# Kernel optimization log

Hardware: AMD Instinct MI355X
Metric: run time of the kernel (lower is better)

Reference implementation:

```python
import jax, jax.numpy as jnp
import numpy as np

B, T, I, H = 64, 512, 1024, 1024


def setup_inputs() -> dict:
    key = jax.random.key(0)
    k1, k2, k3, k4 = jax.random.split(key, 4)
    s_in = 1.0 / np.sqrt(I)
    s_h = 1.0 / np.sqrt(H)
    return {
        "x": jax.random.normal(k1, (B, T, I), dtype=jnp.float32),
        "Wih": jax.random.normal(k2, (4 * H, I), dtype=jnp.float32) * s_in,
        "Whh": jax.random.normal(k3, (4 * H, H), dtype=jnp.float32) * s_h,
        "b": jax.random.normal(k4, (4 * H,), dtype=jnp.float32) * s_h,
    }


def reference(x, Wih, Whh, b):
    """Sequential RNN layer (LSTM cell step) over (batch, seq_len, input).

    Mirrors RNNLayer.forward_tensor: zero-initialized state, per-timestep
    step(), stacked outputs plus final state. The Python time loop is
    expressed as a single lax.scan (one fused launch).
    """
    batch = x.shape[0]
    h0 = jnp.zeros((batch, H), dtype=x.dtype)
    c0 = jnp.zeros((batch, H), dtype=x.dtype)

    def step(carry, xt):  # xt: [B, I]
        h, c = carry
        gates = xt @ Wih.T + h @ Whh.T + b  # [B, 4H]
        i_g, f_g, g_g, o_g = jnp.split(gates, 4, axis=-1)
        c_new = jax.nn.sigmoid(f_g) * c + jax.nn.sigmoid(i_g) * jnp.tanh(g_g)
        h_new = jax.nn.sigmoid(o_g) * jnp.tanh(c_new)
        return (h_new, c_new), h_new

    xs = jnp.swapaxes(x, 0, 1)  # [T, B, I] for scan over time
    (h_T, c_T), outs = jax.lax.scan(step, (h0, c0), xs)
    outputs = jnp.swapaxes(outs, 0, 1)  # [B, T, H]
    return outputs, (h_T, c_T)
```

## Files before the change

kernel.cpp:

```cpp
#include <hip/hip_runtime.h>
#include <stdint.h>


typedef __bf16 bf16x8 __attribute__((ext_vector_type(8)));
typedef float f32x4 __attribute__((ext_vector_type(4)));

#define BATCH 64
#define TSEQ 512
#define HID 1024
#define MROWS (BATCH * TSEQ)
#define NGATE 4096

__device__ __forceinline__ unsigned short f2bf(float f) {
  union { float f; unsigned u; } v; v.f = f;
  unsigned r = (v.u + 0x7FFFu + ((v.u >> 16) & 1u)) >> 16;
  return (unsigned short)r;
}
__device__ __forceinline__ float bf2f(unsigned short u) {
  union { unsigned u; float f; } v; v.u = ((unsigned)u) << 16;
  return v.f;
}

__global__ void cvt_kernel(const float* __restrict__ src,
                           unsigned short* __restrict__ dst, int n4) {
  int i = blockIdx.x * blockDim.x + threadIdx.x;
  const int stride = gridDim.x * blockDim.x;
  for (; i < n4; i += stride) {
    float4 f = ((const float4*)src)[i];
    ushort4 u;
    u.x = f2bf(f.x); u.y = f2bf(f.y); u.z = f2bf(f.z); u.w = f2bf(f.w);
    ((ushort4*)dst)[i] = u;
  }
}

__device__ __forceinline__ void gl_lds16(const unsigned short* g, unsigned short* lds) {
  __builtin_amdgcn_global_load_lds(
      (const __attribute__((address_space(1))) unsigned int*)g,
      (__attribute__((address_space(3))) unsigned int*)lds, 16, 0, 0);
}

__global__ __launch_bounds__(256, 2) void gemm_xg(
    const unsigned short* __restrict__ A,
    const unsigned short* __restrict__ B,
    const float* __restrict__ bias,
    unsigned short* __restrict__ Xg)
{
  __shared__ __align__(16) unsigned short Asm[128 * 32];
  __shared__ __align__(16) unsigned short Bsm[128 * 32];
  const int tid = threadIdx.x;
  const int lane = tid & 63;
  const int wave = tid >> 6;
  const int row0 = blockIdx.y * 128;
  const int col0 = blockIdx.x * 128;
  const int wm = (wave >> 1) * 64;
  const int wn = (wave & 1) * 64;
  const int s_ml = lane >> 2;
  const int s_q = ((lane & 3) ^ (s_ml >> 1)) & 3;
  const int fm = lane & 15;
  const int fq = lane >> 4;
  const int swz = ((fq ^ (fm >> 1)) & 3) * 8;

  f32x4 acc[4][4] = {};

  for (int kt = 0; kt < 32; ++kt) {
    const int k0 = kt * 32;
    __syncthreads();
#pragma unroll
    for (int gI = 0; gI < 2; ++gI) {
      const int grp = wave * 2 + gI;
      const unsigned short* ga =
          A + (size_t)(row0 + grp * 16 + s_ml) * 1024 + k0 + s_q * 8;
      gl_lds16(ga, &Asm[grp * 512]);
      const unsigned short* gb =
          B + (size_t)(col0 + grp * 16 + s_ml) * 1024 + k0 + s_q * 8;
      gl_lds16(gb, &Bsm[grp * 512]);
    }
    __syncthreads();
    bf16x8 af[4], bfv[4];
#pragma unroll
    for (int mt = 0; mt < 4; ++mt) {
      const int m = wm + mt * 16 + fm;
      af[mt] = *(const bf16x8*)&Asm[(m >> 4) * 512 + fm * 32 + swz];
    }
#pragma unroll
    for (int nt = 0; nt < 4; ++nt) {
      const int n = wn + nt * 16 + fm;
      bfv[nt] = *(const bf16x8*)&Bsm[(n >> 4) * 512 + fm * 32 + swz];
    }
#pragma unroll
    for (int mt = 0; mt < 4; ++mt)
#pragma unroll
      for (int nt = 0; nt < 4; ++nt)
        acc[mt][nt] = __builtin_amdgcn_mfma_f32_16x16x32_bf16(
            af[mt], bfv[nt], acc[mt][nt], 0, 0, 0);
  }
#pragma unroll
  for (int nt = 0; nt < 4; ++nt) {
    const int nb = col0 + wn + nt * 16;
    const int pbase = ((nb & 1023) >> 4) * 64 + (nb >> 10) * 16;
    const float bv = bias[nb + fm];
#pragma unroll
    for (int mt = 0; mt < 4; ++mt) {
#pragma unroll
      for (int r = 0; r < 4; ++r) {
        const int row = row0 + wm + mt * 16 + fq * 4 + r;
        Xg[(size_t)row * 4096 + pbase + fm] = f2bf(acc[mt][nt][r] + bv);
      }
    }
  }
}

__device__ __forceinline__ bf16x8 load_h16B(const unsigned short* p) {
  union { unsigned long long q[2]; bf16x8 v; } u;
  const unsigned long long* q = (const unsigned long long*)p;
  u.q[0] = __hip_atomic_load(q, __ATOMIC_RELAXED, __HIP_MEMORY_SCOPE_AGENT);
  u.q[1] = __hip_atomic_load(q + 1, __ATOMIC_RELAXED, __HIP_MEMORY_SCOPE_AGENT);
  return u.v;
}

__global__ __launch_bounds__(256, 1) void lstm_seq(
    const unsigned short* __restrict__ Whh,
    const unsigned short* __restrict__ Xg,
    float* __restrict__ out,
    unsigned short* __restrict__ hbuf,
    unsigned int* __restrict__ flags)
{
  __shared__ float part[4][16][68];
  const int tid = threadIdx.x;
  const int lane = tid & 63;
  const int wave = tid >> 6;
  const int bn = blockIdx.x >> 2;
  const int mi = blockIdx.x & 3;
  const int fm = lane & 15;
  const int fq = lane >> 4;
  unsigned int* flg = flags + mi * 64 * 32;
  unsigned int* myflag = flg + bn * 32;
  unsigned int* pollp = flg + (wave * 16 + (lane & 15)) * 32;

  bf16x8 bfrag[4][8];
#pragma unroll
  for (int g = 0; g < 4; ++g) {
    const unsigned short* wrow =
        Whh + (size_t)(g * 1024 + bn * 16 + fm) * 1024 + wave * 256 + fq * 8;
#pragma unroll
    for (int ki = 0; ki < 8; ++ki) bfrag[g][ki] = *(const bf16x8*)(wrow + ki * 32);
  }

  const int em = tid >> 4, ej = tid & 15;
  const int gb = mi * 16 + em;
  const int gj = bn * 16 + ej;
  float c_reg = 0.f;

  unsigned short* h0 = hbuf;
  unsigned short* h1 = hbuf + BATCH * HID;

  const unsigned short* xrow = Xg + (size_t)gb * TSEQ * 4096 + bn * 64;
  float xpre[4];
#pragma unroll
  for (int g = 0; g < 4; ++g) xpre[g] = bf2f(xrow[g * 16 + ej]);

  for (int t = 0; t < TSEQ; ++t) {
    const unsigned short* hp = (t & 1) ? h1 : h0;
    unsigned short* hn = (t & 1) ? h0 : h1;
    const unsigned short* ab =
        hp + (size_t)(mi * 16 + fm) * 1024 + wave * 256 + fq * 8;

    float xcur[4];
#pragma unroll
    for (int g = 0; g < 4; ++g) xcur[g] = xpre[g];
    if (t < TSEQ - 1) {
      const unsigned short* xn = xrow + (size_t)(t + 1) * 4096;
#pragma unroll
      for (int g = 0; g < 4; ++g) xpre[g] = bf2f(xn[g * 16 + ej]);
    }

    if (t > 0) {
      for (;;) {
        const unsigned f = __hip_atomic_load(pollp, __ATOMIC_RELAXED,
                                             __HIP_MEMORY_SCOPE_AGENT);
        if (__all((int)(f >= (unsigned)t))) break;
        __builtin_amdgcn_s_sleep(1);
      }
      __builtin_amdgcn_sched_barrier(0);
    }

    bf16x8 afr[8];
#pragma unroll
    for (int ki = 0; ki < 8; ++ki) afr[ki] = load_h16B(ab + ki * 32);

    f32x4 acc[4] = {};
#pragma unroll
    for (int ki = 0; ki < 8; ++ki)
#pragma unroll
      for (int g = 0; g < 4; ++g)
        acc[g] = __builtin_amdgcn_mfma_f32_16x16x32_bf16(afr[ki], bfrag[g][ki],
                                                         acc[g], 0, 0, 0);

#pragma unroll
    for (int g = 0; g < 4; ++g)
#pragma unroll
      for (int r = 0; r < 4; ++r)
        part[wave][fq * 4 + r][g * 16 + fm] = acc[g][r];
    __syncthreads();

    float gate[4];
#pragma unroll
    for (int g = 0; g < 4; ++g) {
      float s = part[0][em][g * 16 + ej] + part[1][em][g * 16 + ej] +
                part[2][em][g * 16 + ej] + part[3][em][g * 16 + ej];
      gate[g] = s + xcur[g];
    }
    const float ig = 1.f / (1.f + __expf(-gate[0]));
    const float fg = 1.f / (1.f + __expf(-gate[1]));
    const float gg = 1.f - 2.f / (__expf(2.f * gate[2]) + 1.f);
    const float og = 1.f / (1.f + __expf(-gate[3]));
    c_reg = fg * c_reg + ig * gg;
    const float th = 1.f - 2.f / (__expf(2.f * c_reg) + 1.f);
    const float hv = og * th;

    __hip_atomic_store(&hn[(size_t)gb * HID + gj], f2bf(hv),
                       __ATOMIC_RELAXED, __HIP_MEMORY_SCOPE_AGENT);

    if (t == TSEQ - 1) {
      out[((size_t)gb * TSEQ + t) * HID + gj] = hv;
      out[(size_t)BATCH * TSEQ * HID + (size_t)gb * HID + gj] = hv;
      out[(size_t)BATCH * TSEQ * HID + (size_t)BATCH * HID + (size_t)gb * HID + gj] = c_reg;
      break;
    }

    __syncthreads();
    if (tid == 0)
      __hip_atomic_store(myflag, (unsigned)(t + 1),
                         __ATOMIC_RELAXED, __HIP_MEMORY_SCOPE_AGENT);

    out[((size_t)gb * TSEQ + t) * HID + gj] = hv;
  }
}

extern "C" void kernel_launch(void* const* d_in, const int* in_sizes, int n_in,
                              void* d_out, int out_size, void* d_ws, size_t ws_size,
                              hipStream_t stream) {
  (void)in_sizes; (void)n_in; (void)out_size;
  const float* x   = (const float*)d_in[0];
  const float* Wih = (const float*)d_in[1];
  const float* Whh = (const float*)d_in[2];
  const float* b   = (const float*)d_in[3];
  float* out = (float*)d_out;

  char* ws = (char*)d_ws;
  unsigned short* hbuf   = (unsigned short*)(ws + 1024);
  unsigned short* x_bf   = (unsigned short*)(ws + 263168);
  unsigned short* wih_bf = (unsigned short*)(ws + 263168 + 67108864);
  unsigned short* whh_bf = (unsigned short*)(ws + 263168 + 75497472);
  unsigned short* xg     = (unsigned short*)(ws + 263168 + 83886080);
  unsigned int* flags = (unsigned int*)x_bf;
  const size_t needed = 263168ULL + 83886080ULL + 268435456ULL;
  if (ws_size < needed) return;

  hipMemsetAsync(hbuf, 0, 2 * BATCH * HID * sizeof(unsigned short), stream);

  cvt_kernel<<<2048, 256, 0, stream>>>(x, x_bf, (MROWS * 1024) / 4);
  cvt_kernel<<<512, 256, 0, stream>>>(Wih, wih_bf, (NGATE * 1024) / 4);
  cvt_kernel<<<512, 256, 0, stream>>>(Whh, whh_bf, (NGATE * 1024) / 4);

  dim3 g(32, 256);
  gemm_xg<<<g, 256, 0, stream>>>(x_bf, wih_bf, b, xg);

  hipMemsetAsync(flags, 0, 4 * 64 * 128, stream);

  lstm_seq<<<256, 256, 0, stream>>>(whh_bf, xg, out, hbuf, flags);
}
```

Measured before the change: 2.235 ms.

## Use per-wave flags and double-buffered LDS to drop the second block barrier

Each wave now publishes its own progress flag once its h stores have drained (s_waitcnt vmcnt(0)). This replaces the second __syncthreads plus a single per-block flag. The partial-sum LDS buffer is double-buffered by step parity, so the next step's writes cannot race the previous step's reads without that barrier. The flags are packed densely, so each lane polls one flag instead of strided cache lines, and the s_sleep in the spin loop is removed. The changes aim to cut per-step synchronisation latency in the sequential recurrence. The cost is more polling traffic and contention, since dense flags share cache lines and the spin no longer sleeps.

```diff
diff --git a/kernel.cpp b/kernel.cpp
--- a/kernel.cpp
+++ b/kernel.cpp
@@ -125,7 +125,7 @@
     unsigned short* __restrict__ hbuf,
     unsigned int* __restrict__ flags)
 {
-  __shared__ float part[4][16][68];
+  __shared__ float part[2][4][16][68];
   const int tid = threadIdx.x;
   const int lane = tid & 63;
   const int wave = tid >> 6;
@@ -133,9 +133,9 @@
   const int mi = blockIdx.x & 3;
   const int fm = lane & 15;
   const int fq = lane >> 4;
-  unsigned int* flg = flags + mi * 64 * 32;
-  unsigned int* myflag = flg + bn * 32;
-  unsigned int* pollp = flg + (wave * 16 + (lane & 15)) * 32;
+  unsigned int* flg = flags + mi * 256;
+  unsigned int* myflag = flg + bn * 4 + wave;
+  unsigned int* pollp = flg + wave * 64 + lane;
 
   bf16x8 bfrag[4][8];
 #pragma unroll
@@ -175,11 +175,12 @@
     }
 
     if (t > 0) {
-      for (;;) {
-        const unsigned f = __hip_atomic_load(pollp, __ATOMIC_RELAXED,
-                                             __HIP_MEMORY_SCOPE_AGENT);
-        if (__all((int)(f >= (unsigned)t))) break;
-        __builtin_amdgcn_s_sleep(1);
+      const unsigned tt = (unsigned)t;
+      unsigned f = __hip_atomic_load(pollp, __ATOMIC_RELAXED,
+                                     __HIP_MEMORY_SCOPE_AGENT);
+      while (!__all((int)(f >= tt))) {
+        f = __hip_atomic_load(pollp, __ATOMIC_RELAXED,
+                              __HIP_MEMORY_SCOPE_AGENT);
       }
       __builtin_amdgcn_sched_barrier(0);
     }
@@ -196,18 +197,19 @@
         acc[g] = __builtin_amdgcn_mfma_f32_16x16x32_bf16(afr[ki], bfrag[g][ki],
                                                          acc[g], 0, 0, 0);
 
+    float (*pp)[16][68] = part[t & 1];
 #pragma unroll
     for (int g = 0; g < 4; ++g)
 #pragma unroll
       for (int r = 0; r < 4; ++r)
-        part[wave][fq * 4 + r][g * 16 + fm] = acc[g][r];
+        pp[wave][fq * 4 + r][g * 16 + fm] = acc[g][r];
     __syncthreads();
 
     float gate[4];
 #pragma unroll
     for (int g = 0; g < 4; ++g) {
-      float s = part[0][em][g * 16 + ej] + part[1][em][g * 16 + ej] +
-                part[2][em][g * 16 + ej] + part[3][em][g * 16 + ej];
+      float s = pp[0][em][g * 16 + ej] + pp[1][em][g * 16 + ej] +
+                pp[2][em][g * 16 + ej] + pp[3][em][g * 16 + ej];
       gate[g] = s + xcur[g];
     }
     const float ig = 1.f / (1.f + __expf(-gate[0]));
@@ -228,8 +230,9 @@
       break;
     }
 
-    __syncthreads();
-    if (tid == 0)
+    asm volatile("s_waitcnt vmcnt(0)" ::: "memory");
+    __builtin_amdgcn_sched_barrier(0);
+    if (lane == 0)
       __hip_atomic_store(myflag, (unsigned)(t + 1),
                          __ATOMIC_RELAXED, __HIP_MEMORY_SCOPE_AGENT);
 
@@ -266,7 +269,7 @@
   dim3 g(32, 256);
   gemm_xg<<<g, 256, 0, stream>>>(x_bf, wih_bf, b, xg);
 
-  hipMemsetAsync(flags, 0, 4 * 64 * 128, stream);
+  hipMemsetAsync(flags, 0, 4 * 256 * sizeof(unsigned int), stream);
 
   lstm_seq<<<256, 256, 0, stream>>>(whh_bf, xg, out, hbuf, flags);
 }
```

New measurement: 2.565 ms. +14.7%, slower.
